# Performance work log

Measured on AMD Instinct MI355X. Metric: run time of the kernel, lower is better.

## Reference

```python
import jax, jax.numpy as jnp
import numpy as np

B, S, D, H = 4, 1024, 2048, 16
DH = D // H  # 128
THETA = 10000.0


def setup_inputs() -> dict:
    key = jax.random.key(0)
    k1, k2, k3 = jax.random.split(key, 3)
    std_qkv = np.sqrt(2.0 / (D + 3 * D)).astype(np.float32)
    std_out = np.sqrt(2.0 / (D + D)).astype(np.float32)
    x = jax.random.normal(k1, (B, S, D), jnp.float32)
    w_qkv = jax.random.normal(k2, (D, 3 * D), jnp.float32) * std_qkv
    w_out = jax.random.normal(k3, (D, D), jnp.float32) * std_out
    # matrix-based RoPE table: [max_seq, d_head//2, 2, 2]
    freqs = jnp.arange(S, dtype=jnp.float32)[:, None] / THETA ** (
        2.0 * jnp.arange(DH // 2, dtype=jnp.float32) / DH)[None, :]
    eye = jnp.array([[1.0, 0.0], [0.0, 1.0]], jnp.float32)
    rot = jnp.array([[0.0, -1.0], [1.0, 0.0]], jnp.float32)
    rope_matrix = (jnp.cos(freqs)[:, :, None, None] * eye
                   + jnp.sin(freqs)[:, :, None, None] * rot)
    token_positions = jnp.arange(S, dtype=jnp.int32)
    return {"x": x, "w_qkv": w_qkv, "w_out": w_out,
            "rope_matrix": rope_matrix, "token_positions": token_positions}


def _apply_rope(t, pe):
    # t: [B, H, S, DH]; pe: [S, DH//2, 2, 2] (gathered by token_positions)
    tr = t.reshape(*t.shape[:-1], DH // 2, 2)  # interleaved (even, odd) pairs
    out = jnp.einsum('bhski,skoi->bhsko', tr, pe)
    return out.reshape(t.shape)


def reference(x, w_qkv, w_out, rope_matrix, token_positions):
    qkv = jnp.einsum('bsd,df->bsf', x, w_qkv)          # [B,S,3D]
    q, k, v = jnp.split(qkv, 3, axis=-1)
    to_heads = lambda t: t.reshape(B, S, H, DH).transpose(0, 2, 1, 3)
    q, k, v = to_heads(q), to_heads(k), to_heads(v)    # [B,H,S,DH]
    pe = rope_matrix[token_positions]                  # [S, DH//2, 2, 2]
    q = _apply_rope(q, pe)
    k = _apply_rope(k, pe)
    scores = jnp.einsum('bhqd,bhkd->bhqk', q, k) / np.float32(np.sqrt(DH))
    causal = jnp.tril(jnp.ones((S, S), dtype=bool))
    scores = jnp.where(causal, scores, -jnp.inf)
    attn = jax.nn.softmax(scores, axis=-1)
    ctx = jnp.einsum('bhqk,bhkd->bhqd', attn, v)       # [B,H,S,DH]
    ctx = ctx.transpose(0, 2, 1, 3).reshape(B, S, D)
    return jnp.einsum('bsd,df->bsf', ctx, w_out)
```

## Files before the change

### kernel.cpp

```cpp
#include <hip/hip_runtime.h>
#include <hip/hip_bf16.h>
#include <math.h>

#define Bn 4
#define Sn 1024
#define Dn 2048
#define Hn 16
#define DHn 128
#define BS (Bn * Sn)
#define QKVC (3 * Dn)

typedef __attribute__((ext_vector_type(8))) short short8;
typedef __attribute__((ext_vector_type(4))) float float4v;

__device__ inline unsigned short f2bf(float x) {
  union { float f; unsigned int u; } v; v.f = x;
  unsigned int r = v.u + 0x7fffu + ((v.u >> 16) & 1u);
  return (unsigned short)(r >> 16);
}
__device__ inline float bf2f(unsigned short b) {
  union { unsigned int u; float f; } v; v.u = ((unsigned int)b) << 16;
  return v.f;
}

__device__ __forceinline__ void gload16(const unsigned short* g, unsigned short* l) {
  __builtin_amdgcn_global_load_lds(
      (const __attribute__((address_space(1))) unsigned int*)g,
      (__attribute__((address_space(3))) unsigned int*)l, 16, 0, 0);
}

__device__ void tc_body(const float* __restrict__ w, unsigned short* __restrict__ wT,
                        int K, int N, int bx, int by, int tid,
                        unsigned short (*t)[72]) {
  const int c0 = bx * 64;
  const int r0 = by * 64;
  const int r = tid >> 2;
  const int cb = (tid & 3) * 16;
#pragma unroll
  for (int it = 0; it < 4; ++it) {
    float4 v = *reinterpret_cast<const float4*>(&w[(long)(r0 + r) * N + c0 + cb + 4 * it]);
    t[r][cb + 4 * it + 0] = f2bf(v.x);
    t[r][cb + 4 * it + 1] = f2bf(v.y);
    t[r][cb + 4 * it + 2] = f2bf(v.z);
    t[r][cb + 4 * it + 3] = f2bf(v.w);
  }
  __syncthreads();
  unsigned short o[16];
#pragma unroll
  for (int e = 0; e < 16; ++e) o[e] = t[cb + e][r];
  unsigned short* dst = &wT[(long)(c0 + r) * K + r0 + cb];
  *reinterpret_cast<short8*>(dst) = *reinterpret_cast<short8*>(&o[0]);
  *reinterpret_cast<short8*>(dst + 8) = *reinterpret_cast<short8*>(&o[8]);
}

__global__ __launch_bounds__(256) void prep_all(
    const float* __restrict__ x, const float* __restrict__ w_qkv,
    const float* __restrict__ w_out, unsigned short* __restrict__ x16,
    unsigned short* __restrict__ wqkvT, unsigned short* __restrict__ woutT) {
  __shared__ unsigned short t[64][72];
  const int bid = blockIdx.x;
  const int tid = threadIdx.x;
  if (bid < 4096) {
    const int id = bid * 256 + tid;
    const float4* p = reinterpret_cast<const float4*>(x) + 2 * (size_t)id;
    float4 a = p[0], b = p[1];
    short8 o;
    o[0] = (short)f2bf(a.x); o[1] = (short)f2bf(a.y);
    o[2] = (short)f2bf(a.z); o[3] = (short)f2bf(a.w);
    o[4] = (short)f2bf(b.x); o[5] = (short)f2bf(b.y);
    o[6] = (short)f2bf(b.z); o[7] = (short)f2bf(b.w);
    *reinterpret_cast<short8*>(x16 + 8 * (size_t)id) = o;
  } else if (bid < 7168) {
    const int lb = bid - 4096;
    tc_body(w_qkv, wqkvT, Dn, QKVC, lb % 96, lb / 96, tid, t);
  } else {
    const int lb = bid - 7168;
    tc_body(w_out, woutT, Dn, Dn, lb % 32, lb / 32, tid, t);
  }
}

#define ABUF(buf) ((buf) * 4096)
#define BBUF(buf) (8192 + (buf) * 4096)

#define TILE_MAP()                                                             \
  const int nwg = gridDim.x * gridDim.y;                                       \
  const int bid = blockIdx.y * gridDim.x + blockIdx.x;                         \
  const int swz = (bid & 7) * (nwg >> 3) + (bid >> 3);                         \
  const int t_ = swz & 255, grp_ = swz >> 8;                                   \
  const int m0 = (t_ >> 3) * 128;                                              \
  const int n0 = ((t_ & 7) + grp_ * 8) * 128;

#define GEMM32_LOOP(A_, BT_, K_)                                               \
  STAGE(A_ + (long)m0 * K_, ABUF(0));                                          \
  STAGE(BT_ + (long)n0 * K_, BBUF(0));                                         \
  __syncthreads();                                                             \
  for (int t = 0; t < nt; ++t) {                                               \
    const int cb = t & 1;                                                      \
    if (t + 1 < nt) {                                                          \
      const long To = (long)(t + 1) * 32;                                      \
      STAGE(A_ + (long)m0 * K_ + To, ABUF(cb ^ 1));                            \
      STAGE(BT_ + (long)n0 * K_ + To, BBUF(cb ^ 1));                           \
    }                                                                          \
    short8 afr[4], bfr[4];                                                     \
    _Pragma("unroll") for (int mi = 0; mi < 4; ++mi)                           \
      afr[mi] = *(const short8*)(lds + ABUF(cb) +                              \
          (wr * 64 + mi * 16 + c) * 32 + ((g ^ cg2) << 3));                    \
    _Pragma("unroll") for (int ni = 0; ni < 4; ++ni)                           \
      bfr[ni] = *(const short8*)(lds + BBUF(cb) +                              \
          (wc * 64 + ni * 16 + c) * 32 + ((g ^ cg2) << 3));                    \
    __builtin_amdgcn_s_setprio(1);                                             \
    _Pragma("unroll") for (int mi = 0; mi < 4; ++mi)                           \
      _Pragma("unroll") for (int ni = 0; ni < 4; ++ni)                         \
        acc[mi][ni] = __builtin_amdgcn_mfma_f32_16x16x32_bf16(                 \
            afr[mi], bfr[ni], acc[mi][ni], 0, 0, 0);                           \
    __builtin_amdgcn_s_setprio(0);                                             \
    __syncthreads();                                                           \
  }

__global__ __launch_bounds__(256, 4) void gemm_qkv(
    const unsigned short* __restrict__ A, const unsigned short* __restrict__ BT,
    const float* __restrict__ rope, const int* __restrict__ tpos,
    unsigned short* __restrict__ qR, unsigned short* __restrict__ kR,
    unsigned short* __restrict__ vT, int K) {
  __shared__ unsigned short lds[16384];
  const int tid = threadIdx.x;
  const int wid = tid >> 6, lane = tid & 63;
  const int c = lane & 15, g = lane >> 4;
  const int wr = wid >> 1, wc = wid & 1;
  const int cg2 = (c >> 1) & 3;

  TILE_MAP()

  const int nt = K >> 5;

  float4v acc[4][4];
#pragma unroll
  for (int i = 0; i < 4; ++i)
#pragma unroll
    for (int j = 0; j < 4; ++j) acc[i][j] = (float4v){0.f, 0.f, 0.f, 0.f};

  auto STAGE = [&](const unsigned short* gbase, int sbase) {
#pragma unroll
    for (int j = 0; j < 2; ++j) {
      const int ch = j * 256 + tid;
      const int r = ch >> 2;
      const int wo = (ch & 3) ^ ((r >> 1) & 3);
      gload16(gbase + (long)r * K + wo * 8, lds + sbase + j * 2048 + wid * 512);
    }
  };

  GEMM32_LOOP(A, BT, K)

  const int type = n0 >> 11;
  const int h = (n0 & 2047) >> 7;
  const long bh = (long)((m0 >> 10) * Hn + h);
  const int s0 = m0 & 1023;

  if (type == 2) {
#pragma unroll
    for (int half = 0; half < 2; ++half) {
      if (wr == half) {
#pragma unroll
        for (int mi = 0; mi < 4; ++mi)
#pragma unroll
          for (int ni = 0; ni < 4; ++ni)
#pragma unroll
            for (int j = 0; j < 4; ++j) {
              const int mml = mi * 16 + g * 4 + j;
              const int nn = wc * 64 + ni * 16 + c;
              lds[nn * 72 + mml] = f2bf(acc[mi][ni][j]);
            }
      }
      __syncthreads();
      unsigned short* dst = vT + bh * (long)DHn * Sn + s0 + half * 64;
#pragma unroll
      for (int it = 0; it < 4; ++it) {
        const int cid = it * 256 + tid;
        const int d = cid >> 3;
        const int sl = (cid & 7) * 8;
        short8 v = *reinterpret_cast<const short8*>(lds + d * 72 + sl);
        *reinterpret_cast<short8*>(dst + (long)d * Sn + sl) = v;
      }
      __syncthreads();
    }
  } else {
    unsigned short* base = (type == 0 ? qR : kR) + (bh * Sn + s0) * DHn;
    const float qsc = (type == 0) ? 0.1275174213f : 1.0f;
#pragma unroll
    for (int half = 0; half < 2; ++half) {
      if (wc == half) {
#pragma unroll
        for (int mi = 0; mi < 4; ++mi)
#pragma unroll
          for (int ni = 0; ni < 4; ++ni)
#pragma unroll
            for (int j = 0; j < 4; ++j) {
              const int mm = wr * 64 + mi * 16 + g * 4 + j;
              const int nnl = ni * 16 + c;
              lds[mm * 72 + nnl] = f2bf(acc[mi][ni][j]);
            }
      }
      __syncthreads();
#pragma unroll
      for (int it = 0; it < 4; ++it) {
        const int cid = it * 256 + tid;
        const int r = cid >> 3;
        const int colc = (cid & 7) * 8;
        const int gcol = half * 64 + colc;
        union { short8 v; unsigned short u[8]; } iw, ow;
        iw.v = *reinterpret_cast<const short8*>(lds + r * 72 + colc);
        const int pos = tpos[s0 + r];
        const float4* pe = reinterpret_cast<const float4*>(rope) +
                           (long)pos * 64 + (gcol >> 1);
#pragma unroll
        for (int p = 0; p < 4; ++p) {
          const float4 m2 = pe[p];
          const float xx = bf2f(iw.u[2 * p]), yy = bf2f(iw.u[2 * p + 1]);
          ow.u[2 * p]     = f2bf((m2.x * xx + m2.y * yy) * qsc);
          ow.u[2 * p + 1] = f2bf((m2.z * xx + m2.w * yy) * qsc);
        }
        *reinterpret_cast<short8*>(base + (long)r * DHn + gcol) = ow.v;
      }
      __syncthreads();
    }
  }
}

__global__ __launch_bounds__(256, 4) void gemm_out(
    const unsigned short* __restrict__ A, const unsigned short* __restrict__ BT,
    float* __restrict__ Cout, int N, int K) {
  __shared__ unsigned short lds[16384];
  const int tid = threadIdx.x;
  const int wid = tid >> 6, lane = tid & 63;
  const int c = lane & 15, g = lane >> 4;
  const int wr = wid >> 1, wc = wid & 1;
  const int cg2 = (c >> 1) & 3;

  TILE_MAP()

  const int nt = K >> 5;

  float4v acc[4][4];
#pragma unroll
  for (int i = 0; i < 4; ++i)
#pragma unroll
    for (int j = 0; j < 4; ++j) acc[i][j] = (float4v){0.f, 0.f, 0.f, 0.f};

  auto STAGE = [&](const unsigned short* gbase, int sbase) {
#pragma unroll
    for (int j = 0; j < 2; ++j) {
      const int ch = j * 256 + tid;
      const int r = ch >> 2;
      const int wo = (ch & 3) ^ ((r >> 1) & 3);
      gload16(gbase + (long)r * K + wo * 8, lds + sbase + j * 2048 + wid * 512);
    }
  };

  GEMM32_LOOP(A, BT, K)

#pragma unroll
  for (int mi = 0; mi < 4; ++mi)
#pragma unroll
    for (int ni = 0; ni < 4; ++ni)
#pragma unroll
      for (int j = 0; j < 4; ++j) {
        const int m = m0 + wr * 64 + mi * 16 + g * 4 + j;
        const int n = n0 + wc * 64 + ni * 16 + c;
        Cout[(long)m * N + n] = acc[mi][ni][j];
      }
}
#undef GEMM32_LOOP
#undef TILE_MAP

__global__ __launch_bounds__(256, 2) void attn_mfma(
    const unsigned short* __restrict__ qR, const unsigned short* __restrict__ kR,
    const unsigned short* __restrict__ vTd, unsigned short* __restrict__ ctx) {
  __shared__ unsigned short lds[32768];
  __shared__ unsigned short Ps[4][16][72];
  const int n = blockIdx.x;
  const int qp = (n < 256) ? (7 - (n >> 6)) : ((n - 256) >> 6);
  const int hb = n & 63;
  const int h = hb >> 2, b = hb & 3;
  const int tid = threadIdx.x, wid = tid >> 6, lane = tid & 63;
  const int c = lane & 15, g = lane >> 4, cg7 = c & 7;
  const long bh = (long)(b * Hn + h);
  const unsigned short* kbase = kR + bh * Sn * DHn;
  const unsigned short* vbase = vTd + bh * DHn * Sn;

  short8 qf[2][4];
#pragma unroll
  for (int sub = 0; sub < 2; ++sub) {
    const unsigned short* qrow =
        qR + (bh * Sn + qp * 128 + sub * 64 + wid * 16 + c) * DHn;
#pragma unroll
    for (int kc = 0; kc < 4; ++kc)
      qf[sub][kc] = *reinterpret_cast<const short8*>(qrow + kc * 32 + g * 8);
  }

  auto STAGE = [&](int kt, int buf) {
#pragma unroll
    for (int j = 0; j < 4; ++j) {
      const int ch = j * 256 + tid;
      const int r = ch >> 4, wd = ch & 15;
      const int ws = (wd & 8) | ((wd & 7) ^ (r & 7));
      gload16(kbase + (long)kt * 8192 + r * 128 + ws * 8,
              lds + buf * 8192 + j * 2048 + wid * 512);
    }
#pragma unroll
    for (int j = 0; j < 4; ++j) {
      const int ch = j * 256 + tid;
      const int d = ch >> 3, sw = ch & 7;
      gload16(vbase + (long)d * Sn + kt * 64 + ((sw ^ (d & 7)) << 3),
              lds + 16384 + buf * 8192 + j * 2048 + wid * 512);
    }
  };

  float m[2] = {-INFINITY, -INFINITY}, lsum[2] = {0.f, 0.f};
  float4v otA[8], otB[8];
#pragma unroll
  for (int fd = 0; fd < 8; ++fd) {
    otA[fd] = (float4v){0.f, 0.f, 0.f, 0.f};
    otB[fd] = (float4v){0.f, 0.f, 0.f, 0.f};
  }

  const int ntt = 2 * qp + 2;
  STAGE(0, 0);
  __syncthreads();
  int cur = 0;

  for (int kt = 0; kt < ntt; ++kt) {
    if (kt + 1 < ntt) STAGE(kt + 1, cur ^ 1);

#pragma unroll
    for (int sub = 0; sub < 2; ++sub) {
      if (sub == 0 && kt == ntt - 1) continue;
      float4v* ot = (sub == 0) ? otA : otB;

      float4v scv[4];
#pragma unroll
      for (int f = 0; f < 4; ++f) scv[f] = (float4v){0.f, 0.f, 0.f, 0.f};
      __builtin_amdgcn_s_setprio(1);
#pragma unroll
      for (int f = 0; f < 4; ++f)
#pragma unroll
        for (int kc = 0; kc < 4; ++kc) {
          const int wp = kc * 4 + g;
          const int ws = (wp & 8) | ((wp & 7) ^ cg7);
          short8 kf = *reinterpret_cast<const short8*>(
              lds + cur * 8192 + (f * 16 + c) * 128 + ws * 8);
          scv[f] = __builtin_amdgcn_mfma_f32_16x16x32_bf16(kf, qf[sub][kc],
                                                           scv[f], 0, 0, 0);
        }
      __builtin_amdgcn_s_setprio(0);

      if (kt == 2 * qp + sub) {
        const int qloc = wid * 16 + c;
#pragma unroll
        for (int f = 0; f < 4; ++f)
#pragma unroll
          for (int j = 0; j < 4; ++j)
            if (f * 16 + g * 4 + j > qloc) scv[f][j] = -INFINITY;
      }

      float tmax = -INFINITY;
#pragma unroll
      for (int f = 0; f < 4; ++f)
#pragma unroll
        for (int j = 0; j < 4; ++j) tmax = fmaxf(tmax, scv[f][j]);
      tmax = fmaxf(tmax, __shfl_xor(tmax, 16));
      tmax = fmaxf(tmax, __shfl_xor(tmax, 32));

      float mnew, corr;
      if (__all(tmax <= m[sub] + 8.f)) {
        mnew = m[sub]; corr = 1.f;
      } else {
        mnew = fmaxf(m[sub], tmax);
        corr = exp2f(m[sub] - mnew);
#pragma unroll
        for (int fd = 0; fd < 8; ++fd) ot[fd] *= corr;
      }
      float psum = 0.f;
#pragma unroll
      for (int f = 0; f < 4; ++f)
#pragma unroll
        for (int j = 0; j < 4; ++j) {
          scv[f][j] = exp2f(scv[f][j] - mnew);
          psum += scv[f][j];
        }
      psum += __shfl_xor(psum, 16);
      psum += __shfl_xor(psum, 32);
      lsum[sub] = lsum[sub] * corr + psum;
      m[sub] = mnew;

#pragma unroll
      for (int f = 0; f < 4; ++f) {
        unsigned int lo = (unsigned)f2bf(scv[f][0]) | ((unsigned)f2bf(scv[f][1]) << 16);
        unsigned int hi = (unsigned)f2bf(scv[f][2]) | ((unsigned)f2bf(scv[f][3]) << 16);
        uint2 pk; pk.x = lo; pk.y = hi;
        *reinterpret_cast<uint2*>(&Ps[wid][c][f * 16 + g * 4]) = pk;
      }

      short8 pf0 = *reinterpret_cast<const short8*>(&Ps[wid][c][g * 8]);
      short8 pf1 = *reinterpret_cast<const short8*>(&Ps[wid][c][32 + g * 8]);
      __builtin_amdgcn_s_setprio(1);
#pragma unroll
      for (int fd = 0; fd < 8; ++fd) {
        short8 vf0 = *reinterpret_cast<const short8*>(
            lds + 16384 + cur * 8192 + (fd * 16 + c) * 64 + ((g ^ cg7) << 3));
        short8 vf1 = *reinterpret_cast<const short8*>(
            lds + 16384 + cur * 8192 + (fd * 16 + c) * 64 + (((g + 4) ^ cg7) << 3));
        ot[fd] = __builtin_amdgcn_mfma_f32_16x16x32_bf16(vf0, pf0, ot[fd], 0, 0, 0);
        ot[fd] = __builtin_amdgcn_mfma_f32_16x16x32_bf16(vf1, pf1, ot[fd], 0, 0, 0);
      }
      __builtin_amdgcn_s_setprio(0);
    }

    __syncthreads();
    cur ^= 1;
  }

#pragma unroll
  for (int sub = 0; sub < 2; ++sub) {
    const float4v* ot = (sub == 0) ? otA : otB;
    const float inv = 1.0f / lsum[sub];
    unsigned short* orow =
        ctx + (long)(b * Sn + qp * 128 + sub * 64 + wid * 16 + c) * Dn + h * DHn;
#pragma unroll
    for (int fd = 0; fd < 8; ++fd) {
      const int d = fd * 16 + g * 4;
      uint2 pk;
      pk.x = (unsigned)f2bf(ot[fd][0] * inv) | ((unsigned)f2bf(ot[fd][1] * inv) << 16);
      pk.y = (unsigned)f2bf(ot[fd][2] * inv) | ((unsigned)f2bf(ot[fd][3] * inv) << 16);
      *reinterpret_cast<uint2*>(orow + d) = pk;
    }
  }
}

extern "C" void kernel_launch(void* const* d_in, const int* in_sizes, int n_in,
                              void* d_out, int out_size, void* d_ws, size_t ws_size,
                              hipStream_t stream) {
  const float* x     = (const float*)d_in[0];
  const float* w_qkv = (const float*)d_in[1];
  const float* w_out = (const float*)d_in[2];
  const float* rope  = (const float*)d_in[3];
  const int*   tpos  = (const int*)d_in[4];
  float* out = (float*)d_out;

  unsigned short* x16    = (unsigned short*)d_ws;
  unsigned short* wqkvT  = x16 + (size_t)BS * Dn;
  unsigned short* woutT  = wqkvT + (size_t)Dn * QKVC;
  unsigned short* qR     = woutT + (size_t)Dn * Dn;
  unsigned short* kR     = qR + (size_t)BS * Dn;
  unsigned short* vT16   = kR + (size_t)BS * Dn;
  unsigned short* ctx16  = vT16 + (size_t)BS * Dn;

  prep_all<<<8192, 256, 0, stream>>>(x, w_qkv, w_out, x16, wqkvT, woutT);
  {
    dim3 grid(BS / 128, QKVC / 128);
    gemm_qkv<<<grid, 256, 0, stream>>>(x16, wqkvT, rope, tpos, qR, kR, vT16, Dn);
  }
  attn_mfma<<<512, 256, 0, stream>>>(qR, kR, vT16, ctx16);
  {
    dim3 grid(BS / 128, Dn / 128);
    gemm_out<<<grid, 256, 0, stream>>>(ctx16, woutT, out, Dn, Dn);
  }
}
```

Measured before the change: 238.5 us.

## Widen GEMM K-step to 64 and load B operand directly into registers

The QKV and output GEMMs now step K by 64 per iteration instead of 32. Only the A tile is staged in LDS, using double buffers of 8192 elements and a new 8-way XOR swizzle. The B operand is loaded straight from global memory into double-buffered registers, and the loop is unrolled by two to alternate buffers. This halves the number of barriers and removes LDS traffic for B, at the cost of more registers (launch bounds lowered to 2 waves per SIMD) and possibly uncoalesced global reads of B.

```diff
diff --git a/kernel.cpp b/kernel.cpp
--- a/kernel.cpp
+++ b/kernel.cpp
@@ -79,8 +79,7 @@
   }
 }
 
-#define ABUF(buf) ((buf) * 4096)
-#define BBUF(buf) (8192 + (buf) * 4096)
+#define ABUF(buf) ((buf) * 8192)
 
 #define TILE_MAP()                                                             \
   const int nwg = gridDim.x * gridDim.y;                                       \
@@ -90,34 +89,47 @@
   const int m0 = (t_ >> 3) * 128;                                              \
   const int n0 = ((t_ & 7) + grp_ * 8) * 128;
 
-#define GEMM32_LOOP(A_, BT_, K_)                                               \
-  STAGE(A_ + (long)m0 * K_, ABUF(0));                                          \
-  STAGE(BT_ + (long)n0 * K_, BBUF(0));                                         \
-  __syncthreads();                                                             \
-  for (int t = 0; t < nt; ++t) {                                               \
-    const int cb = t & 1;                                                      \
-    if (t + 1 < nt) {                                                          \
-      const long To = (long)(t + 1) * 32;                                      \
-      STAGE(A_ + (long)m0 * K_ + To, ABUF(cb ^ 1));                            \
-      STAGE(BT_ + (long)n0 * K_ + To, BBUF(cb ^ 1));                           \
-    }                                                                          \
-    short8 afr[4], bfr[4];                                                     \
+#define LOADB(BT_, K_, k0_, bf_)                                               \
+  _Pragma("unroll") for (int ni = 0; ni < 4; ++ni)                             \
+    _Pragma("unroll") for (int ks = 0; ks < 2; ++ks)                           \
+      bf_[ni][ks] = *(const short8*)((BT_) +                                   \
+          (long)(n0 + wc * 64 + ni * 16 + c) * (K_) + (k0_) + (ks * 4 + g) * 8);
+
+#define GEMM_BODY(BUF, BREG)                                                   \
+  {                                                                            \
+    short8 afr[4][2];                                                          \
     _Pragma("unroll") for (int mi = 0; mi < 4; ++mi)                           \
-      afr[mi] = *(const short8*)(lds + ABUF(cb) +                              \
-          (wr * 64 + mi * 16 + c) * 32 + ((g ^ cg2) << 3));                    \
-    _Pragma("unroll") for (int ni = 0; ni < 4; ++ni)                           \
-      bfr[ni] = *(const short8*)(lds + BBUF(cb) +                              \
-          (wc * 64 + ni * 16 + c) * 32 + ((g ^ cg2) << 3));                    \
+      _Pragma("unroll") for (int ks = 0; ks < 2; ++ks)                         \
+        afr[mi][ks] = *(const short8*)(lds + ABUF(BUF) +                       \
+            (wr * 64 + mi * 16 + c) * 64 + (((ks * 4 + g) ^ cg7) << 3));       \
     __builtin_amdgcn_s_setprio(1);                                             \
     _Pragma("unroll") for (int mi = 0; mi < 4; ++mi)                           \
       _Pragma("unroll") for (int ni = 0; ni < 4; ++ni)                         \
-        acc[mi][ni] = __builtin_amdgcn_mfma_f32_16x16x32_bf16(                 \
-            afr[mi], bfr[ni], acc[mi][ni], 0, 0, 0);                           \
+        _Pragma("unroll") for (int ks = 0; ks < 2; ++ks)                       \
+          acc[mi][ni] = __builtin_amdgcn_mfma_f32_16x16x32_bf16(               \
+              afr[mi][ks], BREG[ni][ks], acc[mi][ni], 0, 0, 0);                \
     __builtin_amdgcn_s_setprio(0);                                             \
     __syncthreads();                                                           \
   }
 
-__global__ __launch_bounds__(256, 4) void gemm_qkv(
+#define GEMM128_LOOP(A_, BT_, K_)                                              \
+  short8 b0[4][2], b1[4][2];                                                   \
+  STAGE(A_ + (long)m0 * K_, ABUF(0));                                          \
+  LOADB(BT_, K_, 0, b0)                                                        \
+  __syncthreads();                                                             \
+  for (int t2 = 0; t2 < nt / 2; ++t2) {                                        \
+    const int t = 2 * t2;                                                      \
+    STAGE(A_ + (long)m0 * K_ + (long)(t + 1) * 64, ABUF(1));                   \
+    LOADB(BT_, K_, (long)(t + 1) * 64, b1)                                     \
+    GEMM_BODY(0, b0)                                                           \
+    if (t + 2 < nt) {                                                          \
+      STAGE(A_ + (long)m0 * K_ + (long)(t + 2) * 64, ABUF(0));                 \
+      LOADB(BT_, K_, (long)(t + 2) * 64, b0)                                   \
+    }                                                                          \
+    GEMM_BODY(1, b1)                                                           \
+  }
+
+__global__ __launch_bounds__(256, 2) void gemm_qkv(
     const unsigned short* __restrict__ A, const unsigned short* __restrict__ BT,
     const float* __restrict__ rope, const int* __restrict__ tpos,
     unsigned short* __restrict__ qR, unsigned short* __restrict__ kR,
@@ -127,11 +139,11 @@
   const int wid = tid >> 6, lane = tid & 63;
   const int c = lane & 15, g = lane >> 4;
   const int wr = wid >> 1, wc = wid & 1;
-  const int cg2 = (c >> 1) & 3;
+  const int cg7 = c & 7;
 
   TILE_MAP()
 
-  const int nt = K >> 5;
+  const int nt = K >> 6;
 
   float4v acc[4][4];
 #pragma unroll
@@ -141,15 +153,15 @@
 
   auto STAGE = [&](const unsigned short* gbase, int sbase) {
 #pragma unroll
-    for (int j = 0; j < 2; ++j) {
+    for (int j = 0; j < 4; ++j) {
       const int ch = j * 256 + tid;
-      const int r = ch >> 2;
-      const int wo = (ch & 3) ^ ((r >> 1) & 3);
+      const int r = ch >> 3;
+      const int wo = (ch & 7) ^ (r & 7);
       gload16(gbase + (long)r * K + wo * 8, lds + sbase + j * 2048 + wid * 512);
     }
   };
 
-  GEMM32_LOOP(A, BT, K)
+  GEMM128_LOOP(A, BT, K)
 
   const int type = n0 >> 11;
   const int h = (n0 & 2047) >> 7;
@@ -226,7 +238,7 @@
   }
 }
 
-__global__ __launch_bounds__(256, 4) void gemm_out(
+__global__ __launch_bounds__(256, 2) void gemm_out(
     const unsigned short* __restrict__ A, const unsigned short* __restrict__ BT,
     float* __restrict__ Cout, int N, int K) {
   __shared__ unsigned short lds[16384];
@@ -234,11 +246,11 @@
   const int wid = tid >> 6, lane = tid & 63;
   const int c = lane & 15, g = lane >> 4;
   const int wr = wid >> 1, wc = wid & 1;
-  const int cg2 = (c >> 1) & 3;
+  const int cg7 = c & 7;
 
   TILE_MAP()
 
-  const int nt = K >> 5;
+  const int nt = K >> 6;
 
   float4v acc[4][4];
 #pragma unroll
@@ -248,15 +260,15 @@
 
   auto STAGE = [&](const unsigned short* gbase, int sbase) {
 #pragma unroll
-    for (int j = 0; j < 2; ++j) {
+    for (int j = 0; j < 4; ++j) {
       const int ch = j * 256 + tid;
-      const int r = ch >> 2;
-      const int wo = (ch & 3) ^ ((r >> 1) & 3);
+      const int r = ch >> 3;
+      const int wo = (ch & 7) ^ (r & 7);
       gload16(gbase + (long)r * K + wo * 8, lds + sbase + j * 2048 + wid * 512);
     }
   };
 
-  GEMM32_LOOP(A, BT, K)
+  GEMM128_LOOP(A, BT, K)
 
 #pragma unroll
   for (int mi = 0; mi < 4; ++mi)
@@ -269,7 +281,9 @@
         Cout[(long)m * N + n] = acc[mi][ni][j];
       }
 }
-#undef GEMM32_LOOP
+#undef GEMM128_LOOP
+#undef GEMM_BODY
+#undef LOADB
 #undef TILE_MAP
 
 __global__ __launch_bounds__(256, 2) void attn_mfma(
```

Measured after the change: 374.4 us. 1.57x slower.
